# Performance work log

Measured on AMD Instinct MI355X. Metric: run time of the kernel, lower is better.

The kernel has to match this reference:

```python
import jax, jax.numpy as jnp
import numpy as np

NUM_HEADS = 16
D_MODEL = 1024


def setup_inputs() -> dict:
    key = jax.random.key(0)
    ks = jax.random.split(key, 12)
    B, S, D = 2, 2048, D_MODEL
    scale = 1.0 / np.sqrt(D)
    inp = {
        "query": jax.random.normal(ks[0], (B, S, D), dtype=jnp.float32),
        "key": jax.random.normal(ks[1], (B, S, D), dtype=jnp.float32),
        "value": jax.random.normal(ks[2], (B, S, D), dtype=jnp.float32),
        "mask": jax.random.randint(ks[3], (B, S, S), 0, 2, dtype=jnp.int32),
        # four Linear(d_model, d_model) layers: torch layout W [out, in], y = x @ W.T + b
        "Wq": jax.random.normal(ks[4], (D, D), dtype=jnp.float32) * scale,
        "bq": jnp.zeros((D,), dtype=jnp.float32),
        "Wk": jax.random.normal(ks[5], (D, D), dtype=jnp.float32) * scale,
        "bk": jnp.zeros((D,), dtype=jnp.float32),
        "Wv": jax.random.normal(ks[6], (D, D), dtype=jnp.float32) * scale,
        "bv": jnp.zeros((D,), dtype=jnp.float32),
        "Wo": jax.random.normal(ks[7], (D, D), dtype=jnp.float32) * scale,
        "bo": jnp.zeros((D,), dtype=jnp.float32),
    }
    return inp


def reference(query, key, value, mask, Wq, bq, Wk, bk, Wv, bv, Wo, bo):
    B, S, D = query.shape
    H = NUM_HEADS
    dk = D // H

    def split_heads(x):  # [B,S,D] -> [B,H,S,dk]
        return x.reshape(B, S, H, dk).transpose(0, 2, 1, 3)

    q = split_heads(query @ Wq.T + bq)
    k = split_heads(key @ Wk.T + bk)
    v = split_heads(value @ Wv.T + bv)

    # naive full-score attention, faithful to the original
    scores = jnp.einsum("bhqd,bhkd->bhqk", q, k) / jnp.sqrt(jnp.asarray(dk, q.dtype))
    scores = jnp.where(mask[:, None, :, :] == 0, jnp.asarray(-1e9, scores.dtype), scores)
    probs = jax.nn.softmax(scores, axis=-1)
    attn = jnp.einsum("bhqk,bhkd->bhqd", probs, v)  # [B,H,S,dk]

    out = attn.transpose(0, 2, 1, 3).reshape(B, S, D)
    return out @ Wo.T + bo
```

## Files before the change

kernel.cpp:

```cpp
#include <hip/hip_runtime.h>
#include <hip/hip_bf16.h>

#define NH 16
#define DK 64
#define SEQ 2048
#define DMODEL 1024
#define BATCH 2
#define MROWS (BATCH * SEQ)

using bf16x8 = __attribute__((ext_vector_type(8))) short;
using f32x4  = __attribute__((ext_vector_type(4))) float;

#define NEGI (-1e30f)
#define QSCALE 0.18033688f

static __device__ __forceinline__ unsigned short f2bf(float x) {
  unsigned u = __builtin_bit_cast(unsigned, x);
  u += 0x7fffu + ((u >> 16) & 1u);
  return (unsigned short)(u >> 16);
}
static __device__ __forceinline__ float bf2f(unsigned short h) {
  unsigned u = ((unsigned)h) << 16;
  return __builtin_bit_cast(float, u);
}
static __device__ __forceinline__ unsigned cvtpk(float a, float b) {
  unsigned r;
  asm("v_cvt_pk_bf16_f32 %0, %1, %2" : "=v"(r) : "v"(a), "v"(b));
  return r;
}
static __device__ __forceinline__ void gl_lds16(const unsigned short* g,
                                                unsigned short* l) {
  __builtin_amdgcn_global_load_lds(
      (const __attribute__((address_space(1))) unsigned int*)g,
      (__attribute__((address_space(3))) unsigned int*)l, 16, 0, 0);
}

static __device__ __forceinline__ void conv8(const float* s, unsigned short* d, long i) {
  const float* p = s + i * 8;
  float4 a = *(const float4*)(p);
  float4 b = *(const float4*)(p + 4);
  uint4 u = {cvtpk(a.x, a.y), cvtpk(a.z, a.w), cvtpk(b.x, b.y), cvtpk(b.z, b.w)};
  *(bf16x8*)(d + i * 8) = __builtin_bit_cast(bf16x8, u);
}

__global__ __launch_bounds__(256) void prep(const float* __restrict__ q,
                                            const float* __restrict__ k,
                                            const float* __restrict__ v,
                                            const float* __restrict__ wq,
                                            const float* __restrict__ wk,
                                            const float* __restrict__ wv,
                                            const float* __restrict__ wo,
                                            const float* __restrict__ bq,
                                            const float* __restrict__ bk,
                                            const float* __restrict__ bv,
                                            const float* __restrict__ bo,
                                            const int* __restrict__ mask,
                                            unsigned short* __restrict__ Qc,
                                            unsigned short* __restrict__ Kc,
                                            unsigned short* __restrict__ Vc,
                                            unsigned short* __restrict__ Wqc,
                                            unsigned short* __restrict__ Wkc,
                                            unsigned short* __restrict__ Wvc,
                                            unsigned short* __restrict__ Woc,
                                            unsigned short* __restrict__ bqc,
                                            unsigned short* __restrict__ bkc,
                                            unsigned short* __restrict__ bvc,
                                            unsigned short* __restrict__ boc,
                                            unsigned long long* __restrict__ pm) {
  const int bid = blockIdx.x;
  const int t   = threadIdx.x;
  const long nQKV8 = (long)MROWS * DMODEL / 8;
  const long nW8   = (long)DMODEL * DMODEL / 8;
  if (bid < 1536) {
    int seg = bid >> 9;
    int ib  = bid & 511;
    const float* s = seg == 0 ? q : (seg == 1 ? k : v);
    unsigned short* d = seg == 0 ? Qc : (seg == 1 ? Kc : Vc);
    long i0 = (long)ib * 256 + t;
    for (long i = i0; i < nQKV8; i += 512 * 256) conv8(s, d, i);
  } else if (bid < 2048) {
    int seg = (bid - 1536) >> 7;
    int ib  = (bid - 1536) & 127;
    const float* s = seg == 0 ? wq : (seg == 1 ? wk : (seg == 2 ? wv : wo));
    unsigned short* d = seg == 0 ? Wqc : (seg == 1 ? Wkc : (seg == 2 ? Wvc : Woc));
    long i0 = (long)ib * 256 + t;
    for (long i = i0; i < nW8; i += 128 * 256) conv8(s, d, i);
  } else if (bid < 2560) {
    const int nwords = BATCH * SEQ * (SEQ / 64);
    int wid  = (((bid - 2048) << 8) + t) >> 6;
    int lane = t & 63;
    for (int w = wid; w < nwords; w += 2048) {
      int mv = mask[(long)w * 64 + lane];
      unsigned long long bb = __ballot(mv != 0);
      if (lane == 0) pm[w] = bb;
    }
  } else {
    for (int c = t; c < 512; c += 256) {
      int seg = c >> 7;
      long i  = c & 127;
      const float* s = seg == 0 ? bq : (seg == 1 ? bk : (seg == 2 ? bv : bo));
      unsigned short* d = seg == 0 ? bqc : (seg == 1 ? bkc : (seg == 2 ? bvc : boc));
      conv8(s, d, i);
    }
  }
}

#define BK 32

static __device__ __forceinline__ void gemm_body(const unsigned short* __restrict__ A,
                                                 const unsigned short* __restrict__ W,
                                                 const unsigned short* __restrict__ bias,
                                                 void* __restrict__ Cv,
                                                 int mode, float cscale, int bid,
                                                 unsigned short* Al, unsigned short* Bl) {
  const int t    = threadIdx.x;
  const int lane = t & 63;
  const int w    = t >> 6;
  const int wm   = w >> 1, wn = w & 1;
  const int g    = lane >> 4, lr = lane & 15;
  const int mb   = bid & 31;
  const int nb   = bid >> 5;
  const long Abase = (long)mb * 128 * 1024;
  const long Wbase = (long)nb * 128 * 1024;
  const int srow = lane >> 2;
  const int scol = (lane & 3) << 3;

  f32x4 acc[4][4] = {};

  for (int kt = 0; kt < 1024; kt += BK) {
    __syncthreads();
#pragma unroll
    for (int q = 0; q < 2; ++q) {
      int slab = w * 2 + q;
      int row  = slab * 16 + srow;
      gl_lds16(A + Abase + (long)row * 1024 + kt + scol, Al + slab * 512);
      gl_lds16(W + Wbase + (long)row * 1024 + kt + scol, Bl + slab * 512);
    }
    asm volatile("s_waitcnt vmcnt(0)" ::: "memory");
    __syncthreads();
    bf16x8 af[4], bfr[4];
#pragma unroll
    for (int i = 0; i < 4; ++i) {
      af[i]  = *(const bf16x8*)(&Al[(wm * 64 + i * 16 + lr) * 32 + g * 8]);
      bfr[i] = *(const bf16x8*)(&Bl[(wn * 64 + i * 16 + lr) * 32 + g * 8]);
    }
#pragma unroll
    for (int i = 0; i < 4; ++i)
#pragma unroll
      for (int j = 0; j < 4; ++j)
        acc[i][j] = __builtin_amdgcn_mfma_f32_16x16x32_bf16(af[i], bfr[j], acc[i][j], 0, 0, 0);
  }

#pragma unroll
  for (int j = 0; j < 4; ++j) {
    int n = nb * 128 + wn * 64 + j * 16 + lr;
    float bv = bf2f(bias[n]);
#pragma unroll
    for (int i = 0; i < 4; ++i) {
      int m0 = mb * 128 + wm * 64 + i * 16 + g * 4;
      float v0 = (acc[i][j][0] + bv) * cscale;
      float v1 = (acc[i][j][1] + bv) * cscale;
      float v2 = (acc[i][j][2] + bv) * cscale;
      float v3 = (acc[i][j][3] + bv) * cscale;
      if (mode == 2) {
        int b = m0 >> 11, s0 = m0 & (SEQ - 1);
        int h = n >> 6, d = n & (DK - 1);
        uint2 pk;
        pk.x = (unsigned)f2bf(v0) | ((unsigned)f2bf(v1) << 16);
        pk.y = (unsigned)f2bf(v2) | ((unsigned)f2bf(v3) << 16);
        *(uint2*)(&((unsigned short*)Cv)[((long)(b * NH + h) * DK + d) * SEQ + s0]) = pk;
      } else if (mode == 1) {
        int b = m0 >> 11, s0 = m0 & (SEQ - 1);
        int h = n >> 6, d = n & (DK - 1);
        unsigned short* p = &((unsigned short*)Cv)[(((long)(b * NH + h) * SEQ + s0) << 6) + d];
        p[0] = f2bf(v0); p[64] = f2bf(v1); p[128] = f2bf(v2); p[192] = f2bf(v3);
      } else {
        float* p = &((float*)Cv)[(long)m0 * DMODEL + n];
        p[0] = v0; p[DMODEL] = v1; p[2 * DMODEL] = v2; p[3 * DMODEL] = v3;
      }
    }
  }
}

__global__ __launch_bounds__(256) void qkv_proj(const unsigned short* __restrict__ Aq,
                                                const unsigned short* __restrict__ Ak,
                                                const unsigned short* __restrict__ Av,
                                                const unsigned short* __restrict__ Wq,
                                                const unsigned short* __restrict__ Wk,
                                                const unsigned short* __restrict__ Wv,
                                                const unsigned short* __restrict__ bq,
                                                const unsigned short* __restrict__ bk,
                                                const unsigned short* __restrict__ bv,
                                                unsigned short* __restrict__ Cq,
                                                unsigned short* __restrict__ Ck,
                                                unsigned short* __restrict__ Cv) {
  __shared__ unsigned short Al[128 * 32];
  __shared__ unsigned short Bl[128 * 32];
  int which = blockIdx.x >> 8;
  int bid   = blockIdx.x & 255;
  const unsigned short* A = which == 0 ? Aq : (which == 1 ? Ak : Av);
  const unsigned short* W = which == 0 ? Wq : (which == 1 ? Wk : Wv);
  const unsigned short* b = which == 0 ? bq : (which == 1 ? bk : bv);
  unsigned short* C = which == 0 ? Cq : (which == 1 ? Ck : Cv);
  int   mode  = which == 2 ? 2 : 1;
  float scale = which == 0 ? QSCALE : 1.0f;
  gemm_body(A, W, b, C, mode, scale, bid, Al, Bl);
}

__global__ __launch_bounds__(256) void gemm_out(const unsigned short* __restrict__ A,
                                                const unsigned short* __restrict__ W,
                                                const unsigned short* __restrict__ bias,
                                                float* __restrict__ C) {
  __shared__ unsigned short Al[128 * 32];
  __shared__ unsigned short Bl[128 * 32];
  gemm_body(A, W, bias, C, 0, 1.0f, blockIdx.x, Al, Bl);
}

#define KVB 64
#define LD 72

__global__ __launch_bounds__(256) void attn(const unsigned short* __restrict__ Q,
                                            const unsigned short* __restrict__ K,
                                            const unsigned short* __restrict__ VT,
                                            const unsigned long long* __restrict__ pm,
                                            unsigned short* __restrict__ O) {
  __shared__ unsigned short Kl[KVB * LD];
  __shared__ unsigned short Vt[DK * LD];
  __shared__ unsigned short Pl[4][32 * LD];
  const int t    = threadIdx.x;
  const int lane = t & 63;
  const int w    = t >> 6;
  const int g    = lane >> 4, lr = lane & 15;
  const int bh   = blockIdx.x & 31;
  const int qb   = blockIdx.x >> 5;
  const int b    = bh >> 4, h = bh & 15;
  const long base = (long)bh * SEQ * DK;
  const int q0   = qb * 128 + w * 32;

  const int kr0 = t >> 3,         kc0 = (t & 7) << 3;
  const int kr1 = (256 + t) >> 3, kc1 = kc0;

  bf16x8 qf[2][2];
#pragma unroll
  for (int qh = 0; qh < 2; ++qh) {
    const unsigned short* qp = Q + base + (long)(q0 + qh * 16 + lr) * DK;
    qf[qh][0] = *(const bf16x8*)(qp + g * 8);
    qf[qh][1] = *(const bf16x8*)(qp + 32 + g * 8);
  }
  float mrun[2] = {NEGI, NEGI}, lrun[2] = {0.f, 0.f};
  f32x4 o[2][4] = {};

  bf16x8 kreg0 = *(const bf16x8*)(K + base + (long)kr0 * DK + kc0);
  bf16x8 kreg1 = *(const bf16x8*)(K + base + (long)kr1 * DK + kc1);
  bf16x8 vreg0 = *(const bf16x8*)(VT + base + (long)kr0 * SEQ + kc0);
  bf16x8 vreg1 = *(const bf16x8*)(VT + base + (long)kr1 * SEQ + kc1);

  for (int kt = 0; kt < SEQ / KVB; ++kt) {
    __syncthreads();
    *(bf16x8*)(&Kl[kr0 * LD + kc0]) = kreg0;
    *(bf16x8*)(&Kl[kr1 * LD + kc1]) = kreg1;
    *(bf16x8*)(&Vt[kr0 * LD + kc0]) = vreg0;
    *(bf16x8*)(&Vt[kr1 * LD + kc1]) = vreg1;
    if (kt + 1 < SEQ / KVB) {
      const int kvb = (kt + 1) * KVB;
      kreg0 = *(const bf16x8*)(K + base + (long)(kvb + kr0) * DK + kc0);
      kreg1 = *(const bf16x8*)(K + base + (long)(kvb + kr1) * DK + kc1);
      vreg0 = *(const bf16x8*)(VT + base + (long)kr0 * SEQ + kvb + kc0);
      vreg1 = *(const bf16x8*)(VT + base + (long)kr1 * SEQ + kvb + kc1);
    }
    __syncthreads();

    f32x4 sc[2][4];
#pragma unroll
    for (int c = 0; c < 4; ++c) {
      bf16x8 kf0 = *(const bf16x8*)(&Kl[(c * 16 + lr) * LD + g * 8]);
      bf16x8 kf1 = *(const bf16x8*)(&Kl[(c * 16 + lr) * LD + 32 + g * 8]);
#pragma unroll
      for (int qh = 0; qh < 2; ++qh) {
        f32x4 a = {};
        a = __builtin_amdgcn_mfma_f32_16x16x32_bf16(kf0, qf[qh][0], a, 0, 0, 0);
        a = __builtin_amdgcn_mfma_f32_16x16x32_bf16(kf1, qf[qh][1], a, 0, 0, 0);
        sc[qh][c] = a;
      }
    }

    unsigned short* P = &Pl[w][0];
#pragma unroll
    for (int qh = 0; qh < 2; ++qh) {
      const unsigned long long mw = pm[((long)b * SEQ + q0 + qh * 16 + lr) * 32 + kt];
      float s[4][4];
      float mt = NEGI;
#pragma unroll
      for (int c = 0; c < 4; ++c)
#pragma unroll
        for (int r = 0; r < 4; ++r) {
          int kvi = c * 16 + g * 4 + r;
          float v = ((mw >> kvi) & 1ull) ? sc[qh][c][r] : -1e9f;
          s[c][r] = v;
          mt = fmaxf(mt, v);
        }
      mt = fmaxf(mt, __shfl_xor(mt, 16, 64));
      mt = fmaxf(mt, __shfl_xor(mt, 32, 64));

      int need = __any(mt > mrun[qh] + 5.0f);
      float mn = mrun[qh], corr = 1.0f;
      if (need) { mn = fmaxf(mrun[qh], mt); corr = __builtin_amdgcn_exp2f(mrun[qh] - mn); mrun[qh] = mn; }

      float pf[4][4];
      float rs = 0.f;
#pragma unroll
      for (int c = 0; c < 4; ++c)
#pragma unroll
        for (int r = 0; r < 4; ++r) {
          float p_ = __builtin_amdgcn_exp2f(s[c][r] - mn);
          pf[c][r] = p_;
          rs += p_;
        }
      rs += __shfl_xor(rs, 16, 64);
      rs += __shfl_xor(rs, 32, 64);

      if (need) {
        lrun[qh] = lrun[qh] * corr + rs;
#pragma unroll
        for (int r = 0; r < 4; ++r) {
          float cq = __shfl(corr, (lane >> 4) * 4 + r, 64);
#pragma unroll
          for (int dt = 0; dt < 4; ++dt) o[qh][dt][r] *= cq;
        }
      } else {
        lrun[qh] += rs;
      }

#pragma unroll
      for (int c = 0; c < 4; ++c) {
        uint2 pk;
        pk.x = cvtpk(pf[c][0], pf[c][1]);
        pk.y = cvtpk(pf[c][2], pf[c][3]);
        *(uint2*)(&P[(qh * 16 + lr) * LD + c * 16 + g * 4]) = pk;
      }
    }
    asm volatile("s_waitcnt lgkmcnt(0)" ::: "memory");
    __builtin_amdgcn_sched_barrier(0);

#pragma unroll
    for (int c32 = 0; c32 < 2; ++c32) {
      bf16x8 pf0 = *(const bf16x8*)(&P[lr * LD + c32 * 32 + g * 8]);
      bf16x8 pf1 = *(const bf16x8*)(&P[(16 + lr) * LD + c32 * 32 + g * 8]);
#pragma unroll
      for (int dt = 0; dt < 4; ++dt) {
        bf16x8 vf = *(const bf16x8*)(&Vt[(dt * 16 + lr) * LD + c32 * 32 + g * 8]);
        o[0][dt] = __builtin_amdgcn_mfma_f32_16x16x32_bf16(pf0, vf, o[0][dt], 0, 0, 0);
        o[1][dt] = __builtin_amdgcn_mfma_f32_16x16x32_bf16(pf1, vf, o[1][dt], 0, 0, 0);
      }
    }
    asm volatile("s_waitcnt lgkmcnt(0)" ::: "memory");
    __builtin_amdgcn_sched_barrier(0);
  }
#pragma unroll
  for (int qh = 0; qh < 2; ++qh) {
    float inv = 1.0f / lrun[qh];
#pragma unroll
    for (int r = 0; r < 4; ++r) {
      float iq = __shfl(inv, (lane >> 4) * 4 + r, 64);
      int q = q0 + qh * 16 + g * 4 + r;
      unsigned short* op = O + ((long)(b * SEQ + q) * DMODEL) + h * DK;
#pragma unroll
      for (int dt = 0; dt < 4; ++dt) op[dt * 16 + lr] = f2bf(o[qh][dt][r] * iq);
    }
  }
}

extern "C" void kernel_launch(void* const* d_in, const int* in_sizes, int n_in,
                              void* d_out, int out_size, void* d_ws, size_t ws_size,
                              hipStream_t stream) {
  const int* maskp = (const int*)d_in[3];
  float* out = (float*)d_out;

  char* ws = (char*)d_ws;
  const long MB = 1 << 20;
  unsigned long long* pm = (unsigned long long*)ws;
  unsigned short* Qc  = (unsigned short*)(ws + 1 * MB);
  unsigned short* Kc  = (unsigned short*)(ws + 9 * MB);
  unsigned short* Vc  = (unsigned short*)(ws + 17 * MB);
  unsigned short* Wqc = (unsigned short*)(ws + 25 * MB);
  unsigned short* Wkc = (unsigned short*)(ws + 27 * MB);
  unsigned short* Wvc = (unsigned short*)(ws + 29 * MB);
  unsigned short* Woc = (unsigned short*)(ws + 31 * MB);
  unsigned short* bqc = (unsigned short*)(ws + 33 * MB);
  unsigned short* bkc = (unsigned short*)(ws + 33 * MB + 4096);
  unsigned short* bvc = (unsigned short*)(ws + 33 * MB + 8192);
  unsigned short* boc = (unsigned short*)(ws + 33 * MB + 12288);
  unsigned short* Qb  = (unsigned short*)(ws + 35 * MB);
  unsigned short* Kb  = (unsigned short*)(ws + 43 * MB);
  unsigned short* Vb  = (unsigned short*)(ws + 51 * MB);
  unsigned short* Ab  = (unsigned short*)(ws + 59 * MB);

  prep<<<2561, 256, 0, stream>>>((const float*)d_in[0], (const float*)d_in[1],
                                 (const float*)d_in[2],
                                 (const float*)d_in[4], (const float*)d_in[6],
                                 (const float*)d_in[8], (const float*)d_in[10],
                                 (const float*)d_in[5], (const float*)d_in[7],
                                 (const float*)d_in[9], (const float*)d_in[11],
                                 maskp,
                                 Qc, Kc, Vc, Wqc, Wkc, Wvc, Woc,
                                 bqc, bkc, bvc, boc, pm);

  qkv_proj<<<768, 256, 0, stream>>>(Qc, Kc, Vc, Wqc, Wkc, Wvc,
                                    bqc, bkc, bvc, Qb, Kb, Vb);

  attn<<<BATCH * NH * (SEQ / 128), 256, 0, stream>>>(Qb, Kb, Vb, pm, Ab);

  gemm_out<<<256, 256, 0, stream>>>(Ab, Woc, boc, out);
}
```

Before: 173.5 us.

## Double attention KV tile to 128 and fuse QK MFMA with masking loop

```diff
diff --git a/kernel.cpp b/kernel.cpp
--- a/kernel.cpp
+++ b/kernel.cpp
@@ -216,8 +216,9 @@
   gemm_body(A, W, bias, C, 0, 1.0f, blockIdx.x, Al, Bl);
 }
 
-#define KVB 64
-#define LD 72
+#define KVB 128
+#define LD  72
+#define LD2 136
 
 __global__ __launch_bounds__(256) void attn(const unsigned short* __restrict__ Q,
                                             const unsigned short* __restrict__ K,
@@ -225,8 +226,8 @@
                                             const unsigned long long* __restrict__ pm,
                                             unsigned short* __restrict__ O) {
   __shared__ unsigned short Kl[KVB * LD];
-  __shared__ unsigned short Vt[DK * LD];
-  __shared__ unsigned short Pl[4][32 * LD];
+  __shared__ unsigned short Vt[DK * LD2];
+  __shared__ unsigned short Pl[4][32 * LD2];
   const int t    = threadIdx.x;
   const int lane = t & 63;
   const int w    = t >> 6;
@@ -237,8 +238,8 @@
   const long base = (long)bh * SEQ * DK;
   const int q0   = qb * 128 + w * 32;
 
-  const int kr0 = t >> 3,         kc0 = (t & 7) << 3;
-  const int kr1 = (256 + t) >> 3, kc1 = kc0;
+  const int krr = t >> 3, kcc = (t & 7) << 3;
+  const int vrr = t >> 4, vcc = (t & 15) << 3;
 
   bf16x8 qf[2][2];
 #pragma unroll
@@ -250,55 +251,54 @@
   float mrun[2] = {NEGI, NEGI}, lrun[2] = {0.f, 0.f};
   f32x4 o[2][4] = {};
 
-  bf16x8 kreg0 = *(const bf16x8*)(K + base + (long)kr0 * DK + kc0);
-  bf16x8 kreg1 = *(const bf16x8*)(K + base + (long)kr1 * DK + kc1);
-  bf16x8 vreg0 = *(const bf16x8*)(VT + base + (long)kr0 * SEQ + kc0);
-  bf16x8 vreg1 = *(const bf16x8*)(VT + base + (long)kr1 * SEQ + kc1);
+  bf16x8 kreg[4], vreg[4];
+#pragma unroll
+  for (int p = 0; p < 4; ++p) {
+    kreg[p] = *(const bf16x8*)(K + base + (long)(p * 32 + krr) * DK + kcc);
+    vreg[p] = *(const bf16x8*)(VT + base + (long)(p * 16 + vrr) * SEQ + vcc);
+  }
 
   for (int kt = 0; kt < SEQ / KVB; ++kt) {
     __syncthreads();
-    *(bf16x8*)(&Kl[kr0 * LD + kc0]) = kreg0;
-    *(bf16x8*)(&Kl[kr1 * LD + kc1]) = kreg1;
-    *(bf16x8*)(&Vt[kr0 * LD + kc0]) = vreg0;
-    *(bf16x8*)(&Vt[kr1 * LD + kc1]) = vreg1;
+#pragma unroll
+    for (int p = 0; p < 4; ++p) {
+      *(bf16x8*)(&Kl[(p * 32 + krr) * LD + kcc]) = kreg[p];
+      *(bf16x8*)(&Vt[(p * 16 + vrr) * LD2 + vcc]) = vreg[p];
+    }
     if (kt + 1 < SEQ / KVB) {
       const int kvb = (kt + 1) * KVB;
-      kreg0 = *(const bf16x8*)(K + base + (long)(kvb + kr0) * DK + kc0);
-      kreg1 = *(const bf16x8*)(K + base + (long)(kvb + kr1) * DK + kc1);
-      vreg0 = *(const bf16x8*)(VT + base + (long)kr0 * SEQ + kvb + kc0);
-      vreg1 = *(const bf16x8*)(VT + base + (long)kr1 * SEQ + kvb + kc1);
+#pragma unroll
+      for (int p = 0; p < 4; ++p) {
+        kreg[p] = *(const bf16x8*)(K + base + (long)(kvb + p * 32 + krr) * DK + kcc);
+        vreg[p] = *(const bf16x8*)(VT + base + (long)(p * 16 + vrr) * SEQ + kvb + vcc);
+      }
     }
     __syncthreads();
 
-    f32x4 sc[2][4];
-#pragma unroll
-    for (int c = 0; c < 4; ++c) {
-      bf16x8 kf0 = *(const bf16x8*)(&Kl[(c * 16 + lr) * LD + g * 8]);
-      bf16x8 kf1 = *(const bf16x8*)(&Kl[(c * 16 + lr) * LD + 32 + g * 8]);
-#pragma unroll
-      for (int qh = 0; qh < 2; ++qh) {
+    unsigned short* P = &Pl[w][0];
+#pragma unroll
+    for (int qh = 0; qh < 2; ++qh) {
+      const long prow = ((long)b * SEQ + q0 + qh * 16 + lr) * 32;
+      const unsigned long long mw0 = pm[prow + 2 * kt];
+      const unsigned long long mw1 = pm[prow + 2 * kt + 1];
+      float s[8][4];
+      float mt = NEGI;
+#pragma unroll
+      for (int c = 0; c < 8; ++c) {
+        bf16x8 kf0 = *(const bf16x8*)(&Kl[(c * 16 + lr) * LD + g * 8]);
+        bf16x8 kf1 = *(const bf16x8*)(&Kl[(c * 16 + lr) * LD + 32 + g * 8]);
         f32x4 a = {};
         a = __builtin_amdgcn_mfma_f32_16x16x32_bf16(kf0, qf[qh][0], a, 0, 0, 0);
         a = __builtin_amdgcn_mfma_f32_16x16x32_bf16(kf1, qf[qh][1], a, 0, 0, 0);
-        sc[qh][c] = a;
-      }
-    }
-
-    unsigned short* P = &Pl[w][0];
-#pragma unroll
-    for (int qh = 0; qh < 2; ++qh) {
-      const unsigned long long mw = pm[((long)b * SEQ + q0 + qh * 16 + lr) * 32 + kt];
-      float s[4][4];
-      float mt = NEGI;
-#pragma unroll
-      for (int c = 0; c < 4; ++c)
+        const unsigned long long mw = (c < 4) ? mw0 : mw1;
 #pragma unroll
         for (int r = 0; r < 4; ++r) {
-          int kvi = c * 16 + g * 4 + r;
-          float v = ((mw >> kvi) & 1ull) ? sc[qh][c][r] : -1e9f;
+          int kvi = (c & 3) * 16 + g * 4 + r;
+          float v = ((mw >> kvi) & 1ull) ? a[r] : -1e9f;
           s[c][r] = v;
           mt = fmaxf(mt, v);
         }
+      }
       mt = fmaxf(mt, __shfl_xor(mt, 16, 64));
       mt = fmaxf(mt, __shfl_xor(mt, 32, 64));
 
@@ -306,14 +306,13 @@
       float mn = mrun[qh], corr = 1.0f;
       if (need) { mn = fmaxf(mrun[qh], mt); corr = __builtin_amdgcn_exp2f(mrun[qh] - mn); mrun[qh] = mn; }
 
-      float pf[4][4];
       float rs = 0.f;
 #pragma unroll
-      for (int c = 0; c < 4; ++c)
+      for (int c = 0; c < 8; ++c)
 #pragma unroll
         for (int r = 0; r < 4; ++r) {
           float p_ = __builtin_amdgcn_exp2f(s[c][r] - mn);
-          pf[c][r] = p_;
+          s[c][r] = p_;
           rs += p_;
         }
       rs += __shfl_xor(rs, 16, 64);
@@ -332,23 +331,23 @@
       }
 
 #pragma unroll
-      for (int c = 0; c < 4; ++c) {
+      for (int c = 0; c < 8; ++c) {
         uint2 pk;
-        pk.x = cvtpk(pf[c][0], pf[c][1]);
-        pk.y = cvtpk(pf[c][2], pf[c][3]);
-        *(uint2*)(&P[(qh * 16 + lr) * LD + c * 16 + g * 4]) = pk;
+        pk.x = cvtpk(s[c][0], s[c][1]);
+        pk.y = cvtpk(s[c][2], s[c][3]);
+        *(uint2*)(&P[(qh * 16 + lr) * LD2 + c * 16 + g * 4]) = pk;
       }
     }
     asm volatile("s_waitcnt lgkmcnt(0)" ::: "memory");
     __builtin_amdgcn_sched_barrier(0);
 
 #pragma unroll
-    for (int c32 = 0; c32 < 2; ++c32) {
-      bf16x8 pf0 = *(const bf16x8*)(&P[lr * LD + c32 * 32 + g * 8]);
-      bf16x8 pf1 = *(const bf16x8*)(&P[(16 + lr) * LD + c32 * 32 + g * 8]);
+    for (int c32 = 0; c32 < 4; ++c32) {
+      bf16x8 pf0 = *(const bf16x8*)(&P[lr * LD2 + c32 * 32 + g * 8]);
+      bf16x8 pf1 = *(const bf16x8*)(&P[(16 + lr) * LD2 + c32 * 32 + g * 8]);
 #pragma unroll
       for (int dt = 0; dt < 4; ++dt) {
-        bf16x8 vf = *(const bf16x8*)(&Vt[(dt * 16 + lr) * LD + c32 * 32 + g * 8]);
+        bf16x8 vf = *(const bf16x8*)(&Vt[(dt * 16 + lr) * LD2 + c32 * 32 + g * 8]);
         o[0][dt] = __builtin_amdgcn_mfma_f32_16x16x32_bf16(pf0, vf, o[0][dt], 0, 0, 0);
         o[1][dt] = __builtin_amdgcn_mfma_f32_16x16x32_bf16(pf1, vf, o[1][dt], 0, 0, 0);
       }
```

After: 172.4 us. No clear change (-0.6%).
